# Optimization experiments

Measured on AMD Instinct MI355X. Metric: run time of the kernel, lower is better.

## Reference

```python
import jax, jax.numpy as jnp
import numpy as np

N_NODES = 50000   # number of graph nodes
N_EDGES = 800000  # avg degree 16
D = 128           # in_dim == all hdims -> residual active every layer
L = 3             # len(cfg['hdims'])


def setup_inputs() -> dict:
    key = jax.random.key(0)
    ks = jax.random.split(key, 8)
    scale = 1.0 / np.sqrt(D)
    x = jax.random.normal(ks[0], (N_NODES, D), dtype=jnp.float32)
    edge_index = jax.random.randint(ks[1], (2, N_EDGES), 0, N_NODES, dtype=jnp.int32)
    in_fc_w = jax.random.normal(ks[2], (D, D), dtype=jnp.float32) * scale
    in_fc_b = jnp.zeros((D,), dtype=jnp.float32)
    # GraphConv per layer: lin_rel (with bias) applied to aggregated neighbors,
    # lin_root (no bias) applied to self features. All layers are DxD -> stack.
    w_rel = jax.random.normal(ks[3], (L, D, D), dtype=jnp.float32) * scale
    b_rel = jnp.zeros((L, D), dtype=jnp.float32)
    w_root = jax.random.normal(ks[4], (L, D, D), dtype=jnp.float32) * scale
    return {"x": x, "edge_index": edge_index, "in_fc_w": in_fc_w,
            "in_fc_b": in_fc_b, "w_rel": w_rel, "b_rel": b_rel, "w_root": w_root}


def reference(x, edge_index, in_fc_w, in_fc_b, w_rel, b_rel, w_root):
    src, dst = edge_index[0], edge_index[1]
    h = x @ in_fc_w + in_fc_b                     # in_fc
    for l in range(L):                            # fixed small layer count
        # GraphConv, aggr='add': gather source feats, scatter-add to targets
        agg = jax.ops.segment_sum(h[src], dst, num_segments=N_NODES)  # [N, D]
        out = agg @ w_rel[l] + b_rel[l] + h @ w_root[l]
        out = jax.nn.relu(out)
        h = out + h                               # residual (dims match)
    return h
```

## Files before the change

kernel.cpp:

```cpp
#include <hip/hip_runtime.h>
#include <hip/hip_bf16.h>


constexpr int D = 128;
constexpr int NB_SHIFT = 7;
constexpr int BCAP = 2560;
constexpr int STRIDE = 3456;
constexpr int CHUNK = 2048;
constexpr int NRANGE = 16;

typedef __attribute__((ext_vector_type(8))) short bf16x8;
typedef __attribute__((ext_vector_type(4))) float f32x4;
typedef __attribute__((ext_vector_type(4))) unsigned int u32x4;

__device__ inline unsigned short f2bf(float f) {
    unsigned int u = __builtin_bit_cast(unsigned int, f);
    u += 0x7FFFu + ((u >> 16) & 1u);
    return (unsigned short)(u >> 16);
}
__device__ inline float bf2f(unsigned short v) {
    return __builtin_bit_cast(float, (unsigned int)v << 16);
}
__device__ inline float bf2f_lo(unsigned int v) {
    return __builtin_bit_cast(float, v << 16);
}
__device__ inline float bf2f_hi(unsigned int v) {
    return __builtin_bit_cast(float, v & 0xFFFF0000u);
}

__global__ __launch_bounds__(256) void prep(
    const float* __restrict__ fc_w, const float* __restrict__ w_rel,
    const float* __restrict__ w_root, unsigned short* __restrict__ Wp,
    int* __restrict__ cursor, unsigned short* __restrict__ hb0,
    unsigned short* __restrict__ hb1, int NB, int N, int CSr)
{
    int blk = blockIdx.x;
    if (blk < 56) {
        int idx = blk * 256 + threadIdx.x;
        int mat  = idx >> 11;
        int rem  = idx & 2047;
        int tn   = rem >> 8;
        int ks   = (rem >> 6) & 3;
        int lane = rem & 63;
        const float* w = (mat == 0) ? fc_w
                       : (mat <= 3) ? w_rel  + (size_t)(mat - 1) * D * D
                                    : w_root + (size_t)(mat - 4) * D * D;
        unsigned short* wp = Wp + (size_t)mat * D * D + (size_t)rem * 8;
        int kbase = ks * 32 + (lane >> 4) * 8;
        int col   = tn * 16 + (lane & 15);
        #pragma unroll
        for (int j = 0; j < 8; ++j)
            wp[j] = f2bf(w[(size_t)(kbase + j) * D + col]);
        return;
    }
    blk -= 56;
    const int ncb = (NB + 255) / 256;
    if (blk < ncb) {
        int i = blk * 256 + threadIdx.x;
        if (i < NB) cursor[i] = 0;
        return;
    }
    const int t = threadIdx.x;
    if (t < 64) {
        int c = t >> 4, w = t & 15;
        ((unsigned int*)(hb0 + (size_t)c * CSr + (size_t)N * 32))[w] = 0u;
    } else if (t < 128) {
        int tt = t - 64;
        int c = tt >> 4, w = tt & 15;
        ((unsigned int*)(hb1 + (size_t)c * CSr + (size_t)N * 32))[w] = 0u;
    }
}

__global__ __launch_bounds__(256) void scatter_gemm(
    const int* __restrict__ src, const int* __restrict__ dst,
    unsigned int* __restrict__ entries, int* __restrict__ cursor, int E, int NB, int NS,
    const float* __restrict__ x, const unsigned short* __restrict__ W1p,
    const float* __restrict__ bias, unsigned short* __restrict__ hb_out, int N, int CSr)
{
    const int tid = threadIdx.x;

    if (blockIdx.x < (unsigned)NS) {
        __shared__ unsigned int   stage[CHUNK];
        __shared__ unsigned short bslot[CHUNK];
        __shared__ int lhist[512];
        __shared__ int lscan[512];
        __shared__ int lgbase[512];
        __shared__ int lcur[512];
        __shared__ int sh[256];

        const int base  = blockIdx.x * CHUNK;
        const int count = min(CHUNK, E - base);

        for (int i = tid; i < 512; i += 256) { lhist[i] = 0; lcur[i] = 0; }
        __syncthreads();

        for (int i = tid; i < count; i += 256)
            atomicAdd(&lhist[dst[base + i] >> NB_SHIFT], 1);
        __syncthreads();

        int v2 = lhist[2 * tid] + lhist[2 * tid + 1];
        sh[tid] = v2;
        __syncthreads();
        #pragma unroll
        for (int off = 1; off < 256; off <<= 1) {
            int t = (tid >= off) ? sh[tid - off] : 0;
            __syncthreads();
            sh[tid] += t;
            __syncthreads();
        }
        int excl2 = sh[tid] - v2;
        lscan[2 * tid]     = excl2;
        lscan[2 * tid + 1] = excl2 + lhist[2 * tid];
        __syncthreads();

        for (int t = tid; t < 512; t += 256) {
            int c = (t < NB) ? lhist[t] : 0;
            lgbase[t] = (c > 0) ? atomicAdd(&cursor[t], c) : 0;
        }
        __syncthreads();

        for (int i = tid; i < count; i += 256) {
            int d = dst[base + i];
            int s = src[base + i];
            int b = d >> NB_SHIFT;
            int p = atomicAdd(&lcur[b], 1);
            int slot = lscan[b] + p;
            stage[slot] = ((unsigned int)(d & ((1 << NB_SHIFT) - 1)) << 16) | (unsigned int)s;
            bslot[slot] = (unsigned short)b;
        }
        __syncthreads();

        for (int i = tid; i < count; i += 256) {
            int b   = bslot[i];
            int off = i - lscan[b] + lgbase[b];
            if (off < BCAP) entries[(size_t)b * BCAP + off] = stage[i];
        }
        return;
    }

    const int blk  = blockIdx.x - NS;
    const int wave = tid >> 6;
    const int lane = tid & 63;
    const int row0 = blk * 64 + wave * 16;
    const int mrow = lane & 15;
    const int kgrp = lane >> 4;

    f32x4 acc[8];
    #pragma unroll
    for (int t = 0; t < 8; ++t) acc[t] = (f32x4){0.f, 0.f, 0.f, 0.f};

    int arow = row0 + mrow; if (arow >= N) arow = N - 1;
    const float* xr = x + (size_t)arow * D + kgrp * 8;

    #pragma unroll
    for (int ks = 0; ks < 4; ++ks) {
        float4 f0 = *(const float4*)(xr + ks * 32);
        float4 f1 = *(const float4*)(xr + ks * 32 + 4);
        bf16x8 a1;
        a1[0] = (short)f2bf(f0.x); a1[1] = (short)f2bf(f0.y);
        a1[2] = (short)f2bf(f0.z); a1[3] = (short)f2bf(f0.w);
        a1[4] = (short)f2bf(f1.x); a1[5] = (short)f2bf(f1.y);
        a1[6] = (short)f2bf(f1.z); a1[7] = (short)f2bf(f1.w);
        #pragma unroll
        for (int tn = 0; tn < 8; ++tn) {
            bf16x8 b = *(const bf16x8*)(W1p + ((size_t)((tn * 4 + ks) * 64 + lane) * 8));
            acc[tn] = __builtin_amdgcn_mfma_f32_16x16x32_bf16(a1, b, acc[tn], 0, 0, 0);
        }
    }

    const int r0 = row0 + kgrp * 4;
    #pragma unroll
    for (int tn = 0; tn < 8; ++tn) {
        const int col = tn * 16 + mrow;
        const float bv = bias[col];
        const int c  = col >> 5;
        const int cc = col & 31;
        #pragma unroll
        for (int reg = 0; reg < 4; ++reg) {
            int r = r0 + reg;
            if (r < N)
                hb_out[(size_t)c * CSr + (size_t)r * 32 + cc] = f2bf(acc[tn][reg] + bv);
        }
    }
}

__global__ __launch_bounds__(256) void bucket_sort(
    const unsigned int* __restrict__ entries, const int* __restrict__ cursor,
    unsigned short* __restrict__ sorted_src, int* __restrict__ eb,
    int N, int NB, float inv_range, int zero_id)
{
    const int b   = blockIdx.x;
    const int tid = threadIdx.x;

    __shared__ int nhist[128 * NRANGE];
    __shared__ int nscan[128 * NRANGE];
    __shared__ int ncur[128 * NRANGE];
    __shared__ int nbase[129];
    __shared__ int sh[256];
    __shared__ unsigned short svals[STRIDE];

    const int cnt = min(cursor[b], BCAP);

    for (int i = tid; i < 128 * NRANGE; i += 256) { nhist[i] = 0; ncur[i] = 0; }
    __syncthreads();

    const unsigned int* ebase = entries + (size_t)b * BCAP;
    for (int i = tid; i < cnt; i += 256) {
        unsigned int e = ebase[i];
        int s = (int)(e & 0xFFFFu);
        int r = (int)((float)s * inv_range); if (r > NRANGE - 1) r = NRANGE - 1;
        atomicAdd(&nhist[(int)((e >> 16) << 4) | r], 1);
    }
    __syncthreads();

    int c4 = 0, pc = 0;
    if (tid < 128) {
        int s = 0;
        #pragma unroll
        for (int q = 0; q < NRANGE; ++q) s += nhist[NRANGE * tid + q];
        c4 = s;
        pc = (c4 + 7) & ~7;
    }
    sh[tid] = (tid < 128) ? pc : 0;
    __syncthreads();
    #pragma unroll
    for (int off = 1; off < 128; off <<= 1) {
        int t = (tid >= off && tid < 128) ? sh[tid - off] : 0;
        __syncthreads();
        if (tid < 128) sh[tid] += t;
        __syncthreads();
    }
    if (tid < 128) nbase[tid] = sh[tid] - pc;
    if (tid == 127) nbase[128] = sh[127];
    __syncthreads();
    const int padded_total = nbase[128];

    if (tid < 128) {
        int base = nbase[tid];
        int run = base;
        #pragma unroll
        for (int q = 0; q < NRANGE; ++q) {
            nscan[NRANGE * tid + q] = run;
            run += nhist[NRANGE * tid + q];
        }
        int nn = (b << NB_SHIFT) + tid;
        if (nn < N) {
            eb[2 * nn]     = b * STRIDE + base;
            eb[2 * nn + 1] = b * STRIDE + base + pc;
        }
    }
    for (int i = tid; i < padded_total; i += 256) svals[i] = (unsigned short)zero_id;
    __syncthreads();

    for (int i = tid; i < cnt; i += 256) {
        unsigned int e = ebase[i];
        int s = (int)(e & 0xFFFFu);
        int r = (int)((float)s * inv_range); if (r > NRANGE - 1) r = NRANGE - 1;
        int key = (int)((e >> 16) << 4) | r;
        int p = atomicAdd(&ncur[key], 1);
        svals[nscan[key] + p] = (unsigned short)s;
    }
    __syncthreads();

    unsigned short* obase = sorted_src + (size_t)b * STRIDE;
    for (int i = tid; i < padded_total; i += 256) obase[i] = svals[i];
}

__global__ __launch_bounds__(256) void gather8(
    const unsigned short* __restrict__ hb_in, const int* __restrict__ eb,
    const unsigned short* __restrict__ sorted_src,
    unsigned short* __restrict__ aggb, int N, int CSr)
{
    const int tid   = threadIdx.x;
    const int chunk = blockIdx.x & 3;
    const int tile  = blockIdx.x >> 2;
    const int lane  = tid & 63;
    const int wave  = tid >> 6;
    const int g     = lane >> 2;
    const int sub   = lane & 3;
    const int n     = tile * 64 + wave * 16 + g;

    const unsigned short* hbc = hb_in + (size_t)chunk * CSr;
    const unsigned int sub8 = (unsigned int)sub * 8;

    float acc[8];
    #pragma unroll
    for (int q = 0; q < 8; ++q) acc[q] = 0.f;

    if (n < N) {
        const int2 be = ((const int2*)eb)[n];
        int j = be.x;
        const int e = be.y;
        if (j < e) {
            u32x4 I = *(const u32x4*)(sorted_src + j);
            for (;;) {
                unsigned int s0 = I[0] & 0xFFFFu, s1 = I[0] >> 16;
                unsigned int s2 = I[1] & 0xFFFFu, s3 = I[1] >> 16;
                unsigned int s4 = I[2] & 0xFFFFu, s5 = I[2] >> 16;
                unsigned int s6 = I[3] & 0xFFFFu, s7 = I[3] >> 16;
                u32x4 v0 = *(const u32x4*)(hbc + (size_t)s0 * 32 + sub8);
                u32x4 v1 = *(const u32x4*)(hbc + (size_t)s1 * 32 + sub8);
                u32x4 v2 = *(const u32x4*)(hbc + (size_t)s2 * 32 + sub8);
                u32x4 v3 = *(const u32x4*)(hbc + (size_t)s3 * 32 + sub8);
                u32x4 v4 = *(const u32x4*)(hbc + (size_t)s4 * 32 + sub8);
                u32x4 v5 = *(const u32x4*)(hbc + (size_t)s5 * 32 + sub8);
                u32x4 v6 = *(const u32x4*)(hbc + (size_t)s6 * 32 + sub8);
                u32x4 v7 = *(const u32x4*)(hbc + (size_t)s7 * 32 + sub8);
                const bool more = (j + 8 < e);
                u32x4 nI;
                if (more) nI = *(const u32x4*)(sorted_src + j + 8);
                #pragma unroll
                for (int q = 0; q < 4; ++q) {
                    acc[2 * q]     += ((bf2f_lo(v0[q]) + bf2f_lo(v1[q])) + (bf2f_lo(v2[q]) + bf2f_lo(v3[q])))
                                    + ((bf2f_lo(v4[q]) + bf2f_lo(v5[q])) + (bf2f_lo(v6[q]) + bf2f_lo(v7[q])));
                    acc[2 * q + 1] += ((bf2f_hi(v0[q]) + bf2f_hi(v1[q])) + (bf2f_hi(v2[q]) + bf2f_hi(v3[q])))
                                    + ((bf2f_hi(v4[q]) + bf2f_hi(v5[q])) + (bf2f_hi(v6[q]) + bf2f_hi(v7[q])));
                }
                if (!more) break;
                I = nI; j += 8;
            }
        }
        u32x4 o;
        #pragma unroll
        for (int q = 0; q < 4; ++q)
            o[q] = (unsigned int)f2bf(acc[2 * q]) |
                   ((unsigned int)f2bf(acc[2 * q + 1]) << 16);
        *(u32x4*)(aggb + (size_t)n * D + chunk * 32 + sub8) = o;
    }
}

__global__ __launch_bounds__(256) void gemm_epi(
    const unsigned short* __restrict__ aggb, const unsigned short* __restrict__ hb_in,
    const unsigned short* __restrict__ Wrel, const unsigned short* __restrict__ Wroot,
    const float* __restrict__ bias, unsigned short* hb_out, float* out_f32,
    int N, int CSr)
{
    const int tid  = threadIdx.x;
    const int wave = tid >> 6;
    const int lane = tid & 63;
    const int row0 = blockIdx.x * 64 + wave * 16;
    const int mrow = lane & 15;
    const int kgrp = lane >> 4;

    f32x4 acc[8];
    #pragma unroll
    for (int t = 0; t < 8; ++t) acc[t] = (f32x4){0.f, 0.f, 0.f, 0.f};

    int arow = row0 + mrow; if (arow >= N) arow = N - 1;
    const unsigned short* ag = aggb + (size_t)arow * D + kgrp * 8;

    #pragma unroll
    for (int ks = 0; ks < 4; ++ks) {
        bf16x8 a1 = *(const bf16x8*)(ag + ks * 32);
        bf16x8 a2 = *(const bf16x8*)(hb_in + (size_t)ks * CSr + (size_t)arow * 32 + kgrp * 8);
        #pragma unroll
        for (int tn = 0; tn < 8; ++tn) {
            bf16x8 b1 = *(const bf16x8*)(Wrel  + ((size_t)((tn * 4 + ks) * 64 + lane) * 8));
            acc[tn] = __builtin_amdgcn_mfma_f32_16x16x32_bf16(a1, b1, acc[tn], 0, 0, 0);
            bf16x8 b2 = *(const bf16x8*)(Wroot + ((size_t)((tn * 4 + ks) * 64 + lane) * 8));
            acc[tn] = __builtin_amdgcn_mfma_f32_16x16x32_bf16(a2, b2, acc[tn], 0, 0, 0);
        }
    }

    const int r0 = row0 + kgrp * 4;
    #pragma unroll
    for (int tn = 0; tn < 8; ++tn) {
        const int col = tn * 16 + mrow;
        const float bv = bias[col];
        const int c  = col >> 5;
        const int cc = col & 31;
        #pragma unroll
        for (int reg = 0; reg < 4; ++reg) {
            int r = r0 + reg;
            if (r < N) {
                float z = fmaxf(acc[tn][reg] + bv, 0.f);
                float o = z + bf2f(hb_in[(size_t)c * CSr + (size_t)r * 32 + cc]);
                if (out_f32 != nullptr) out_f32[(size_t)r * D + col] = o;
                else hb_out[(size_t)c * CSr + (size_t)r * 32 + cc] = f2bf(o);
            }
        }
    }
}

extern "C" void kernel_launch(void* const* d_in, const int* in_sizes, int n_in,
                              void* d_out, int out_size, void* d_ws, size_t ws_size,
                              hipStream_t stream)
{
    const float* x      = (const float*)d_in[0];
    const int*   ei     = (const int*)  d_in[1];
    const float* fc_w   = (const float*)d_in[2];
    const float* fc_b   = (const float*)d_in[3];
    const float* w_rel  = (const float*)d_in[4];
    const float* b_rel  = (const float*)d_in[5];
    const float* w_root = (const float*)d_in[6];
    float* out = (float*)d_out;

    const int N = in_sizes[0] / D;
    const int E = in_sizes[1] / 2;
    const int* src = ei;
    const int* dst = ei + E;
    const int NB = (N + (1 << NB_SHIFT) - 1) >> NB_SHIFT;
    const int CSr = (N + 1) * 32;

    char* p = (char*)d_ws;
    unsigned short* hb0  = (unsigned short*)p;  p += (size_t)4 * CSr * sizeof(unsigned short);
    unsigned short* hb1  = (unsigned short*)p;  p += (size_t)4 * CSr * sizeof(unsigned short);
    unsigned short* aggb = (unsigned short*)p;  p += (size_t)N * D * sizeof(unsigned short);
    unsigned short* Wp   = (unsigned short*)p;  p += (size_t)7 * D * D * sizeof(unsigned short);
    unsigned short* sorted_src = (unsigned short*)p;  p += (size_t)NB * STRIDE * sizeof(unsigned short);
    int* eb     = (int*)p;                      p += (size_t)2 * N * sizeof(int);
    int* cursor = (int*)p;                      p += (size_t)NB * sizeof(int);
    unsigned int* entries = (unsigned int*)d_out;

    unsigned short* Wp_in   = Wp;
    unsigned short* Wp_rel  = Wp + (size_t)1 * D * D;
    unsigned short* Wp_root = Wp + (size_t)4 * D * D;

    const int NS = (E + CHUNK - 1) / CHUNK;
    const int gemm_blocks   = (N + 63) / 64;
    const int tiles         = (N + 63) / 64;
    const int prep_blocks   = 56 + (NB + 255) / 256 + 1;

    prep<<<prep_blocks, 256, 0, stream>>>(fc_w, w_rel, w_root, Wp, cursor,
                                          hb0, hb1, NB, N, CSr);

    scatter_gemm<<<NS + gemm_blocks, 256, 0, stream>>>(
        src, dst, entries, cursor, E, NB, NS,
        x, Wp_in, fc_b, hb0, N, CSr);

    bucket_sort<<<NB, 256, 0, stream>>>(
        entries, cursor, sorted_src, eb, N, NB, (float)NRANGE / (float)N, N);

    unsigned short* hin  = hb0;
    unsigned short* hout = hb1;
    for (int l = 0; l < 3; ++l) {
        gather8<<<tiles * 4, 256, 0, stream>>>(hin, eb, sorted_src, aggb, N, CSr);
        gemm_epi<<<gemm_blocks, 256, 0, stream>>>(
            aggb, hin,
            Wp_rel + (size_t)l * D * D, Wp_root + (size_t)l * D * D,
            b_rel + (size_t)l * D,
            (l == 2) ? nullptr : hout,
            (l == 2) ? out : nullptr, N, CSr);
        unsigned short* t = hin; hin = hout; hout = t;
    }
}
```

Before: 247.5 us.

## Transform before aggregating: GEMM first, then gather transformed rows with fused epilogue

Uses linearity of segment_sum to compute h@W_rel and h@W_root+b first, then gathers the transformed rows and applies relu plus residual in the gather kernel. This drops the separate aggregated buffer and the second GEMM input read. It writes two bf16 intermediates per layer instead, adding traffic. The gather is also restructured so four lanes split the edges of each node, with shuffle reductions. An extra bf16 rounding of the transformed rows before summation may shift numerics slightly.

```diff
diff --git a/kernel.cpp b/kernel.cpp
--- a/kernel.cpp
+++ b/kernel.cpp
@@ -31,8 +31,8 @@
 __global__ __launch_bounds__(256) void prep(
     const float* __restrict__ fc_w, const float* __restrict__ w_rel,
     const float* __restrict__ w_root, unsigned short* __restrict__ Wp,
-    int* __restrict__ cursor, unsigned short* __restrict__ hb0,
-    unsigned short* __restrict__ hb1, int NB, int N, int CSr)
+    int* __restrict__ cursor, unsigned short* __restrict__ hrb,
+    int NB, int N, int CSr)
 {
     int blk = blockIdx.x;
     if (blk < 56) {
@@ -63,11 +63,7 @@
     const int t = threadIdx.x;
     if (t < 64) {
         int c = t >> 4, w = t & 15;
-        ((unsigned int*)(hb0 + (size_t)c * CSr + (size_t)N * 32))[w] = 0u;
-    } else if (t < 128) {
-        int tt = t - 64;
-        int c = tt >> 4, w = tt & 15;
-        ((unsigned int*)(hb1 + (size_t)c * CSr + (size_t)N * 32))[w] = 0u;
+        ((unsigned int*)(hrb + (size_t)c * CSr + (size_t)N * 32))[w] = 0u;
     }
 }
 
@@ -266,73 +262,11 @@
     for (int i = tid; i < padded_total; i += 256) obase[i] = svals[i];
 }
 
-__global__ __launch_bounds__(256) void gather8(
-    const unsigned short* __restrict__ hb_in, const int* __restrict__ eb,
-    const unsigned short* __restrict__ sorted_src,
-    unsigned short* __restrict__ aggb, int N, int CSr)
-{
-    const int tid   = threadIdx.x;
-    const int chunk = blockIdx.x & 3;
-    const int tile  = blockIdx.x >> 2;
-    const int lane  = tid & 63;
-    const int wave  = tid >> 6;
-    const int g     = lane >> 2;
-    const int sub   = lane & 3;
-    const int n     = tile * 64 + wave * 16 + g;
-
-    const unsigned short* hbc = hb_in + (size_t)chunk * CSr;
-    const unsigned int sub8 = (unsigned int)sub * 8;
-
-    float acc[8];
-    #pragma unroll
-    for (int q = 0; q < 8; ++q) acc[q] = 0.f;
-
-    if (n < N) {
-        const int2 be = ((const int2*)eb)[n];
-        int j = be.x;
-        const int e = be.y;
-        if (j < e) {
-            u32x4 I = *(const u32x4*)(sorted_src + j);
-            for (;;) {
-                unsigned int s0 = I[0] & 0xFFFFu, s1 = I[0] >> 16;
-                unsigned int s2 = I[1] & 0xFFFFu, s3 = I[1] >> 16;
-                unsigned int s4 = I[2] & 0xFFFFu, s5 = I[2] >> 16;
-                unsigned int s6 = I[3] & 0xFFFFu, s7 = I[3] >> 16;
-                u32x4 v0 = *(const u32x4*)(hbc + (size_t)s0 * 32 + sub8);
-                u32x4 v1 = *(const u32x4*)(hbc + (size_t)s1 * 32 + sub8);
-                u32x4 v2 = *(const u32x4*)(hbc + (size_t)s2 * 32 + sub8);
-                u32x4 v3 = *(const u32x4*)(hbc + (size_t)s3 * 32 + sub8);
-                u32x4 v4 = *(const u32x4*)(hbc + (size_t)s4 * 32 + sub8);
-                u32x4 v5 = *(const u32x4*)(hbc + (size_t)s5 * 32 + sub8);
-                u32x4 v6 = *(const u32x4*)(hbc + (size_t)s6 * 32 + sub8);
-                u32x4 v7 = *(const u32x4*)(hbc + (size_t)s7 * 32 + sub8);
-                const bool more = (j + 8 < e);
-                u32x4 nI;
-                if (more) nI = *(const u32x4*)(sorted_src + j + 8);
-                #pragma unroll
-                for (int q = 0; q < 4; ++q) {
-                    acc[2 * q]     += ((bf2f_lo(v0[q]) + bf2f_lo(v1[q])) + (bf2f_lo(v2[q]) + bf2f_lo(v3[q])))
-                                    + ((bf2f_lo(v4[q]) + bf2f_lo(v5[q])) + (bf2f_lo(v6[q]) + bf2f_lo(v7[q])));
-                    acc[2 * q + 1] += ((bf2f_hi(v0[q]) + bf2f_hi(v1[q])) + (bf2f_hi(v2[q]) + bf2f_hi(v3[q])))
-                                    + ((bf2f_hi(v4[q]) + bf2f_hi(v5[q])) + (bf2f_hi(v6[q]) + bf2f_hi(v7[q])));
-                }
-                if (!more) break;
-                I = nI; j += 8;
-            }
-        }
-        u32x4 o;
-        #pragma unroll
-        for (int q = 0; q < 4; ++q)
-            o[q] = (unsigned int)f2bf(acc[2 * q]) |
-                   ((unsigned int)f2bf(acc[2 * q + 1]) << 16);
-        *(u32x4*)(aggb + (size_t)n * D + chunk * 32 + sub8) = o;
-    }
-}
-
-__global__ __launch_bounds__(256) void gemm_epi(
-    const unsigned short* __restrict__ aggb, const unsigned short* __restrict__ hb_in,
+__global__ __launch_bounds__(256) void gemm_dual(
+    const unsigned short* __restrict__ hb_in,
     const unsigned short* __restrict__ Wrel, const unsigned short* __restrict__ Wroot,
-    const float* __restrict__ bias, unsigned short* hb_out, float* out_f32,
+    const float* __restrict__ bias,
+    unsigned short* __restrict__ hr_out, unsigned short* __restrict__ hro_out,
     int N, int CSr)
 {
     const int tid  = threadIdx.x;
@@ -342,23 +276,24 @@
     const int mrow = lane & 15;
     const int kgrp = lane >> 4;
 
-    f32x4 acc[8];
-    #pragma unroll
-    for (int t = 0; t < 8; ++t) acc[t] = (f32x4){0.f, 0.f, 0.f, 0.f};
+    f32x4 accR[8], accO[8];
+    #pragma unroll
+    for (int t = 0; t < 8; ++t) {
+        accR[t] = (f32x4){0.f, 0.f, 0.f, 0.f};
+        accO[t] = (f32x4){0.f, 0.f, 0.f, 0.f};
+    }
 
     int arow = row0 + mrow; if (arow >= N) arow = N - 1;
-    const unsigned short* ag = aggb + (size_t)arow * D + kgrp * 8;
 
     #pragma unroll
     for (int ks = 0; ks < 4; ++ks) {
-        bf16x8 a1 = *(const bf16x8*)(ag + ks * 32);
-        bf16x8 a2 = *(const bf16x8*)(hb_in + (size_t)ks * CSr + (size_t)arow * 32 + kgrp * 8);
+        bf16x8 a = *(const bf16x8*)(hb_in + (size_t)ks * CSr + (size_t)arow * 32 + kgrp * 8);
         #pragma unroll
         for (int tn = 0; tn < 8; ++tn) {
             bf16x8 b1 = *(const bf16x8*)(Wrel  + ((size_t)((tn * 4 + ks) * 64 + lane) * 8));
-            acc[tn] = __builtin_amdgcn_mfma_f32_16x16x32_bf16(a1, b1, acc[tn], 0, 0, 0);
+            accR[tn] = __builtin_amdgcn_mfma_f32_16x16x32_bf16(a, b1, accR[tn], 0, 0, 0);
             bf16x8 b2 = *(const bf16x8*)(Wroot + ((size_t)((tn * 4 + ks) * 64 + lane) * 8));
-            acc[tn] = __builtin_amdgcn_mfma_f32_16x16x32_bf16(a2, b2, acc[tn], 0, 0, 0);
+            accO[tn] = __builtin_amdgcn_mfma_f32_16x16x32_bf16(a, b2, accO[tn], 0, 0, 0);
         }
     }
 
@@ -373,12 +308,91 @@
         for (int reg = 0; reg < 4; ++reg) {
             int r = r0 + reg;
             if (r < N) {
-                float z = fmaxf(acc[tn][reg] + bv, 0.f);
-                float o = z + bf2f(hb_in[(size_t)c * CSr + (size_t)r * 32 + cc]);
-                if (out_f32 != nullptr) out_f32[(size_t)r * D + col] = o;
-                else hb_out[(size_t)c * CSr + (size_t)r * 32 + cc] = f2bf(o);
+                hr_out [(size_t)c * CSr + (size_t)r * 32 + cc] = f2bf(accR[tn][reg]);
+                hro_out[(size_t)c * CSr + (size_t)r * 32 + cc] = f2bf(accO[tn][reg] + bv);
             }
         }
+    }
+}
+
+__global__ __launch_bounds__(256) void gather_epi(
+    const unsigned short* __restrict__ hr, const unsigned short* __restrict__ hro,
+    const unsigned short* __restrict__ hb_in,
+    const int* __restrict__ eb, const unsigned short* __restrict__ sorted_src,
+    unsigned short* hb_out, float* out_f32, int N, int CSr)
+{
+    const int tid   = threadIdx.x;
+    const int chunk = blockIdx.x & 3;
+    const int tile  = blockIdx.x >> 2;
+    const int wave  = tid >> 6;
+    const int lane  = tid & 63;
+    const int g     = lane >> 4;
+    const int es    = (lane >> 2) & 3;
+    const int cs    = lane & 3;
+    const int n     = tile * 16 + wave * 4 + g;
+
+    const unsigned short* hrc = hr + (size_t)chunk * CSr;
+    const unsigned int cs8 = (unsigned int)cs * 8;
+
+    float acc[8];
+    #pragma unroll
+    for (int q = 0; q < 8; ++q) acc[q] = 0.f;
+
+    if (n >= N) return;
+
+    const int2 be = ((const int2*)eb)[n];
+    int j = be.x;
+    const int e = be.y;
+
+    if (j < e) {
+        unsigned int ids = *(const unsigned int*)(sorted_src + j + 2 * es);
+        for (;;) {
+            unsigned int s0 = ids & 0xFFFFu;
+            unsigned int s1 = ids >> 16;
+            u32x4 v0 = *(const u32x4*)(hrc + (size_t)s0 * 32 + cs8);
+            u32x4 v1 = *(const u32x4*)(hrc + (size_t)s1 * 32 + cs8);
+            const bool more = (j + 8 < e);
+            unsigned int nids;
+            if (more) nids = *(const unsigned int*)(sorted_src + j + 8 + 2 * es);
+            #pragma unroll
+            for (int q = 0; q < 4; ++q) {
+                acc[2 * q]     += bf2f_lo(v0[q]) + bf2f_lo(v1[q]);
+                acc[2 * q + 1] += bf2f_hi(v0[q]) + bf2f_hi(v1[q]);
+            }
+            if (!more) break;
+            ids = nids; j += 8;
+        }
+        #pragma unroll
+        for (int q = 0; q < 8; ++q) {
+            acc[q] += __shfl_xor(acc[q], 4);
+            acc[q] += __shfl_xor(acc[q], 8);
+        }
+    }
+
+    if (es != 0) return;
+
+    const size_t roff = (size_t)chunk * CSr + (size_t)n * 32 + cs8;
+    u32x4 ro = *(const u32x4*)(hro + roff);
+    u32x4 hv = *(const u32x4*)(hb_in + roff);
+
+    float o[8];
+    #pragma unroll
+    for (int q = 0; q < 4; ++q) {
+        o[2 * q]     = fmaxf(acc[2 * q]     + bf2f_lo(ro[q]), 0.f) + bf2f_lo(hv[q]);
+        o[2 * q + 1] = fmaxf(acc[2 * q + 1] + bf2f_hi(ro[q]), 0.f) + bf2f_hi(hv[q]);
+    }
+
+    if (out_f32 != nullptr) {
+        float* op = out_f32 + (size_t)n * D + chunk * 32 + cs * 8;
+        *(float4*)(op)     = (float4){o[0], o[1], o[2], o[3]};
+        *(float4*)(op + 4) = (float4){o[4], o[5], o[6], o[7]};
+    } else {
+        u32x4 ov;
+        #pragma unroll
+        for (int q = 0; q < 4; ++q)
+            ov[q] = (unsigned int)f2bf(o[2 * q]) |
+                    ((unsigned int)f2bf(o[2 * q + 1]) << 16);
+        *(u32x4*)(hb_out + roff) = ov;
     }
 }
 
@@ -403,13 +417,14 @@
     const int CSr = (N + 1) * 32;
 
     char* p = (char*)d_ws;
-    unsigned short* hb0  = (unsigned short*)p;  p += (size_t)4 * CSr * sizeof(unsigned short);
-    unsigned short* hb1  = (unsigned short*)p;  p += (size_t)4 * CSr * sizeof(unsigned short);
-    unsigned short* aggb = (unsigned short*)p;  p += (size_t)N * D * sizeof(unsigned short);
-    unsigned short* Wp   = (unsigned short*)p;  p += (size_t)7 * D * D * sizeof(unsigned short);
+    unsigned short* hb0 = (unsigned short*)p;  p += (size_t)4 * CSr * sizeof(unsigned short);
+    unsigned short* hb1 = (unsigned short*)p;  p += (size_t)4 * CSr * sizeof(unsigned short);
+    unsigned short* hrb = (unsigned short*)p;  p += (size_t)4 * CSr * sizeof(unsigned short);
+    unsigned short* hob = (unsigned short*)p;  p += (size_t)4 * CSr * sizeof(unsigned short);
+    unsigned short* Wp  = (unsigned short*)p;  p += (size_t)7 * D * D * sizeof(unsigned short);
     unsigned short* sorted_src = (unsigned short*)p;  p += (size_t)NB * STRIDE * sizeof(unsigned short);
-    int* eb     = (int*)p;                      p += (size_t)2 * N * sizeof(int);
-    int* cursor = (int*)p;                      p += (size_t)NB * sizeof(int);
+    int* eb     = (int*)p;                     p += (size_t)2 * N * sizeof(int);
+    int* cursor = (int*)p;                     p += (size_t)NB * sizeof(int);
     unsigned int* entries = (unsigned int*)d_out;
 
     unsigned short* Wp_in   = Wp;
@@ -417,12 +432,12 @@
     unsigned short* Wp_root = Wp + (size_t)4 * D * D;
 
     const int NS = (E + CHUNK - 1) / CHUNK;
-    const int gemm_blocks   = (N + 63) / 64;
-    const int tiles         = (N + 63) / 64;
-    const int prep_blocks   = 56 + (NB + 255) / 256 + 1;
+    const int gemm_blocks = (N + 63) / 64;
+    const int tiles16     = (N + 15) / 16;
+    const int prep_blocks = 56 + (NB + 255) / 256 + 1;
 
     prep<<<prep_blocks, 256, 0, stream>>>(fc_w, w_rel, w_root, Wp, cursor,
-                                          hb0, hb1, NB, N, CSr);
+                                          hrb, NB, N, CSr);
 
     scatter_gemm<<<NS + gemm_blocks, 256, 0, stream>>>(
         src, dst, entries, cursor, E, NB, NS,
@@ -434,11 +449,13 @@
     unsigned short* hin  = hb0;
     unsigned short* hout = hb1;
     for (int l = 0; l < 3; ++l) {
-        gather8<<<tiles * 4, 256, 0, stream>>>(hin, eb, sorted_src, aggb, N, CSr);
-        gemm_epi<<<gemm_blocks, 256, 0, stream>>>(
-            aggb, hin,
+        gemm_dual<<<gemm_blocks, 256, 0, stream>>>(
+            hin,
             Wp_rel + (size_t)l * D * D, Wp_root + (size_t)l * D * D,
             b_rel + (size_t)l * D,
+            hrb, hob, N, CSr);
+        gather_epi<<<tiles16 * 4, 256, 0, stream>>>(
+            hrb, hob, hin, eb, sorted_src,
             (l == 2) ? nullptr : hout,
             (l == 2) ? out : nullptr, N, CSr);
         unsigned short* t = hin; hin = hout; hout = t;
```

Result: slower. 257.6 us (+4.1%).
